# Optimization experiments

Hardware: AMD Instinct MI355X
Metric: run time of the kernel (lower is better)

The kernel has to match this reference:

```python
import jax, jax.numpy as jnp
from jax import lax
import numpy as np

DC = 3.79
HSTEP = 0.1
EPS = 1e-5
BIG = 1e10

def conv1(x, K):
    p = (K.shape[-1] - 1) // 2
    return lax.conv_general_dilated(x, K, (1,), [(p, p)], dimension_numbers=("NCH", "OIH", "NCH"))

def conv1T(x, K):
    # conv_transpose1d(stride=1, padding=p) == conv1d with flipped kernel and swapped in/out channels
    return conv1(x, jnp.flip(jnp.swapaxes(K, 0, 1), -1))

def masked_instance_norm(x, mask, eps=EPS):
    denom = jnp.sum(mask, axis=2, keepdims=True)
    mean = jnp.sum(x * mask, axis=2, keepdims=True) / denom
    meanm = mean * mask  # original multiplies the broadcast mean by the mask
    var = jnp.sum(((x - meanm) * mask) ** 2, axis=2, keepdims=True) / denom
    return (x - meanm) / jnp.sqrt(var + eps)

def avg_pool3s2(x):
    # torch avg_pool1d(kernel=3, stride=2, padding=1, count_include_pad=True)
    s = lax.reduce_window(x, 0.0, lax.add, (1, 1, 3), (1, 1, 2), [(0, 0), (0, 0), (1, 1)])
    return s / 3.0

def dist_constraint(X, M_fixed, M_padding, dc=DC):
    # X: [nb,3,n]; M_fixed, M_padding: [nb,1,n]. Vectorized (scan) version of the
    # original per-segment python loops: left/right propagation from fixed anchors
    # via unit-step (length dc) cumulative sums, blended by distance weights.
    dX = X[:, :, 1:] - X[:, :, :-1]
    d = jnp.sum(dX * dX, axis=1, keepdims=True)  # [nb,1,n-1]
    avM = jnp.floor((M_padding[..., 1:] + M_padding[..., :-1]) / 2.0) < 0.5
    dXn = dX / jnp.sqrt(d + avM) * jnp.where(avM, 0.0, dc)  # [nb,3,n-1]
    fixed = M_fixed[:, 0, :] == 1  # [nb,n]

    Xt = jnp.moveaxis(X, 2, 0)      # [n,nb,3]
    dXnt = jnp.moveaxis(dXn, 2, 0)  # [n-1,nb,3]
    ft = fixed.T                    # [n,nb]

    def lstep(carry, inp):
        prev, seen, wl = carry
        xj, dxn, fj = inp
        val = jnp.where(fj[:, None] | ~seen[:, None], xj, prev + dxn)
        wl2 = (wl + 1.0) * (~fj)
        return (val, seen | fj, wl2), (val, wl2)

    wl0 = jnp.where(ft[0], 0.0, BIG)
    _, (lv, lw) = lax.scan(lstep, (Xt[0], ft[0], wl0), (Xt[1:], dXnt, ft[1:]))
    Xleft = jnp.concatenate([X[:, :, :1], jnp.moveaxis(lv, 0, 2)], axis=2)
    wl = jnp.concatenate([wl0[:, None], lw.T], axis=1)  # [nb,n]

    def rstep(carry, inp):
        nxt, seen, wr = carry
        xj, dxn, fj = inp
        val = jnp.where(fj[:, None] | ~seen[:, None], xj, nxt - dxn)
        wr2 = (wr + 1.0) * (~fj)
        return (val, seen | fj, wr2), (val, wr2)

    wrN = jnp.where(ft[-1], 0.0, BIG)
    _, (rv, rw) = lax.scan(rstep, (Xt[-1], ft[-1], wrN), (Xt[:-1], dXnt, ft[:-1]), reverse=True)
    Xright = jnp.concatenate([jnp.moveaxis(rv, 0, 2), X[:, :, -1:]], axis=2)
    wr = jnp.concatenate([rw.T, wrN[:, None]], axis=1)

    ws = wl + wr
    ws_safe = jnp.where(ws == 0.0, 1.0, ws)
    cl = jnp.where(ws == 0.0, 0.5, wr / ws_safe)  # weight on Xleft = (wsum-wl)/wsum
    cr = jnp.where(ws == 0.0, 0.5, wl / ws_safe)
    X2 = Xleft * cl[:, None, :] + Xright * cr[:, None, :]
    return X2 * M_padding

def tr2dist(Y):
    # pairwise Euclidean distances from coords [nb,3,n] -> [nb,n,n]
    Z = jnp.swapaxes(Y, 1, 2)
    Z = Z - jnp.mean(Z, axis=1, keepdims=True)
    sq = jnp.sum(Z * Z, axis=2)
    D2 = sq[:, :, None] + sq[:, None, :] - 2.0 * jnp.einsum("bic,bjc->bij", Z, Z)
    return jnp.sqrt(jnp.maximum(D2, 0.0) + 1e-8)

def vnet_forward(x, mask, Ks, W):
    coords = x[:, -4:-1, :]
    mask_coords = jnp.repeat((x[:, -1, :] == 1)[:, None, :], 3, axis=1)
    m = mask[:, None, :]
    nL = len(Ks)
    xc = jax.nn.relu(masked_instance_norm(conv1(x, Ks[0]) * m, m))  # dropout_p=0 -> identity
    xS, mS = [], []
    for i in range(1, nL):
        K = Ks[i]
        if K.shape[0] == K.shape[1]:
            z = jax.nn.relu(masked_instance_norm(conv1(xc, K) * m, m))
            xc = xc - HSTEP * (conv1T(z, K) * m)
        else:
            xS.append(xc)
            xc = jax.nn.relu(masked_instance_norm(conv1(xc, K) * m, m))
            mS.append(m)
            m = (avg_pool3s2(m) >= 0.5).astype(x.dtype)
            xc = avg_pool3s2(xc) * m
    ns = len(xS)
    for i in reversed(range(1, nL)):
        K = Ks[i]
        if K.shape[0] == K.shape[1]:
            z = jax.nn.relu(masked_instance_norm(conv1T(xc, K) * m, m))
            xc = xc - HSTEP * (conv1(z, K) * m)
        else:
            ns -= 1
            m = mS[ns]
            xc = jnp.repeat(xc, 2, axis=-1) * m  # F.interpolate(scale=2, mode='nearest')
            z = masked_instance_norm(conv1T(xc, K) * m, m)
            xc = jax.nn.relu(z) + xS[ns]
    xc = conv1(xc, W) * m
    xc = jnp.where(mask_coords, coords, xc)
    xout = dist_constraint(xc, mask_coords[:, :1, :].astype(x.dtype), m)
    return tr2dist(xout), xout

def setup_inputs() -> dict:
    key = jax.random.key(0)
    ks = jax.random.split(key, 12)
    nb, n = 8, 2048
    feats = jax.random.normal(ks[0], (nb, 20, n), dtype=jnp.float32)
    coords = jax.random.normal(ks[1], (nb, 3, n), dtype=jnp.float32)
    lengths = jax.random.randint(ks[2], (nb,), n // 2, n + 1)
    mask = (jnp.arange(n)[None, :] < lengths[:, None]).astype(jnp.float32)  # ragged padding mask
    flag = (jax.random.uniform(ks[3], (nb, n)) < 0.5).astype(jnp.float32) * mask  # fixed-coord flag
    x = jnp.concatenate([feats, coords, flag[:, None, :]], axis=1)

    def unif(k, shape, stdv):
        return jax.random.uniform(k, shape, jnp.float32, -stdv, stdv)

    K0 = unif(ks[4], (32, 24, 3), 0.1 * 24 / 32)
    K1 = unif(ks[5], (32, 32, 3), 0.01)
    K2 = unif(ks[6], (32, 32, 3), 0.01)
    K3 = unif(ks[7], (64, 32, 3), 0.1 * 32 / 64)
    K4 = unif(ks[8], (64, 64, 3), 0.01)
    K5 = unif(ks[9], (64, 64, 3), 0.01)
    K6 = unif(ks[10], (128, 64, 3), 0.1 * 64 / 128)
    W = 0.1 * jax.random.normal(ks[11], (3, 32, 1), dtype=jnp.float32)
    return {"x": x, "mask": mask, "K0": K0, "K1": K1, "K2": K2, "K3": K3, "K4": K4, "K5": K5, "K6": K6, "W": W}

def reference(x, mask, K0, K1, K2, K3, K4, K5, K6, W):
    dists, xout = vnet_forward(x, mask, [K0, K1, K2, K3, K4, K5, K6], W)
    return (dists, xout)
```

## Files before the change

### kernel.cpp

```cpp
#include <hip/hip_runtime.h>
#include <math.h>

#define HSTEP 0.1f
#define EPS_IN 1e-5f
#define BIGF 1e10f
#define DCF 3.79f

__device__ inline float block_sum1(float v, float* sred) {
    #pragma unroll
    for (int off = 32; off > 0; off >>= 1) v += __shfl_down(v, off);
    int wid = threadIdx.x >> 6;
    int nw  = blockDim.x >> 6;
    if ((threadIdx.x & 63) == 0) sred[wid] = v;
    __syncthreads();
    float total = 0.f;
    for (int i = 0; i < nw; ++i) total += sred[i];
    __syncthreads();
    return total;
}

__device__ inline float2 block_sum2(float a, float b, float2* sred) {
    #pragma unroll
    for (int off = 32; off > 0; off >>= 1) {
        a += __shfl_down(a, off);
        b += __shfl_down(b, off);
    }
    int wid = threadIdx.x >> 6;
    int nw  = blockDim.x >> 6;
    if ((threadIdx.x & 63) == 0) sred[wid] = make_float2(a, b);
    __syncthreads();
    float ta = 0.f, tb = 0.f;
    for (int i = 0; i < nw; ++i) { ta += sred[i].x; tb += sred[i].y; }
    __syncthreads();
    return make_float2(ta, tb);
}

template<int CIN, bool TR>
__global__ void __launch_bounds__(1024)
conv_in_relu_kernel(const float* __restrict__ xin, float* __restrict__ out,
                    const float* __restrict__ K, int Cout, int N,
                    const float* __restrict__ mask, const float* __restrict__ denom,
                    const float* __restrict__ skip)
{
    __shared__ float srow[2048];
    __shared__ float swt[CIN * 3];
    __shared__ float2 sred[16];

    const int b   = blockIdx.x / Cout;
    const int co  = blockIdx.x % Cout;
    const int tid = threadIdx.x;

    for (int i = tid; i < CIN * 3; i += blockDim.x) {
        int ci = i / 3, k = i % 3;
        swt[i] = TR ? K[((size_t)ci * Cout + co) * 3 + (2 - k)]
                    : K[((size_t)co * CIN + ci) * 3 + k];
    }
    __syncthreads();

    const float* mrow = mask + (size_t)b * N;
    const float* xb   = xin + (size_t)b * CIN * N;
    float lsum = 0.f, lss = 0.f;
    for (int n = tid; n < N; n += 1024) {
        float acc = 0.f;
        const float* xr = xb + n;
        #pragma unroll 8
        for (int ci = 0; ci < CIN; ++ci, xr += N) {
            float xm = (n > 0)     ? xr[-1] : 0.f;
            float x0 = xr[0];
            float xp = (n < N - 1) ? xr[1]  : 0.f;
            acc = fmaf(swt[ci * 3 + 0], xm, acc);
            acc = fmaf(swt[ci * 3 + 1], x0, acc);
            acc = fmaf(swt[ci * 3 + 2], xp, acc);
        }
        float v = acc * mrow[n];
        srow[n] = v;
        lsum += v;
        lss  += v * v;
    }
    float dn = denom[b];
    float2 s = block_sum2(lsum, lss, sred);
    float mean = s.x / dn;
    float var  = s.y / dn - mean * mean;
    float inv  = 1.f / sqrtf(var + EPS_IN);

    float* orow = out + ((size_t)b * Cout + co) * N;
    const float* skrow = skip ? skip + ((size_t)b * Cout + co) * N : nullptr;
    for (int n = tid; n < N; n += 1024) {
        float mk = mrow[n];
        float zv = (srow[n] - mean * mk) * inv;
        float r  = fmaxf(zv, 0.f);
        if (skrow) r += skrow[n];
        orow[n] = r;
    }
}

template<int CIN, bool TR>
__global__ void __launch_bounds__(1024)
conv_axpy_kernel(const float* __restrict__ z, float* __restrict__ xc,
                 const float* __restrict__ K, int Cout, int N,
                 const float* __restrict__ mask)
{
    __shared__ float swt[CIN * 3];
    const int b   = blockIdx.x / Cout;
    const int co  = blockIdx.x % Cout;
    const int tid = threadIdx.x;

    for (int i = tid; i < CIN * 3; i += blockDim.x) {
        int ci = i / 3, k = i % 3;
        swt[i] = TR ? K[((size_t)ci * Cout + co) * 3 + (2 - k)]
                    : K[((size_t)co * CIN + ci) * 3 + k];
    }
    __syncthreads();

    const float* mrow = mask + (size_t)b * N;
    const float* zb   = z + (size_t)b * CIN * N;
    float* orow = xc + ((size_t)b * Cout + co) * N;
    for (int n = tid; n < N; n += 1024) {
        float acc = 0.f;
        const float* zr = zb + n;
        #pragma unroll 8
        for (int ci = 0; ci < CIN; ++ci, zr += N) {
            float xm = (n > 0)     ? zr[-1] : 0.f;
            float x0 = zr[0];
            float xp = (n < N - 1) ? zr[1]  : 0.f;
            acc = fmaf(swt[ci * 3 + 0], xm, acc);
            acc = fmaf(swt[ci * 3 + 1], x0, acc);
            acc = fmaf(swt[ci * 3 + 2], xp, acc);
        }
        orow[n] -= HSTEP * acc * mrow[n];
    }
}

__global__ void __launch_bounds__(256)
mask_prep_kernel(const float* __restrict__ mask, float* __restrict__ M1,
                 float* __restrict__ M2, float* __restrict__ d0, float* __restrict__ d1)
{
    __shared__ float sm1[1024];
    __shared__ float sredf[4];
    int b = blockIdx.x, tid = threadIdx.x;
    const float* mr = mask + (size_t)b * 2048;

    float s0 = 0.f;
    for (int n = tid; n < 2048; n += 256) s0 += mr[n];
    float t0 = block_sum1(s0, sredf);
    if (tid == 0) d0[b] = t0;

    for (int n = tid; n < 1024; n += 256) {
        float s = mr[2 * n];
        if (2 * n - 1 >= 0)   s += mr[2 * n - 1];
        if (2 * n + 1 < 2048) s += mr[2 * n + 1];
        float v = (s * (1.f / 3.f) >= 0.5f) ? 1.f : 0.f;
        sm1[n] = v;
        M1[(size_t)b * 1024 + n] = v;
    }
    __syncthreads();
    float s1 = 0.f;
    for (int n = tid; n < 1024; n += 256) s1 += sm1[n];
    float t1 = block_sum1(s1, sredf);
    if (tid == 0) d1[b] = t1;

    for (int n = tid; n < 512; n += 256) {
        float s = sm1[2 * n];
        if (2 * n - 1 >= 0)   s += sm1[2 * n - 1];
        if (2 * n + 1 < 1024) s += sm1[2 * n + 1];
        M2[(size_t)b * 512 + n] = (s * (1.f / 3.f) >= 0.5f) ? 1.f : 0.f;
    }
}

__global__ void pool_x_kernel(const float* __restrict__ xin, float* __restrict__ xout,
                              const float* __restrict__ mnew, int C, int Nin, int Nout, int B)
{
    int idx = blockIdx.x * blockDim.x + threadIdx.x;
    if (idx >= B * C * Nout) return;
    int n  = idx % Nout;
    int bc = idx / Nout;
    int b  = bc / C;
    const float* r = xin + (size_t)bc * Nin;
    float s = r[2 * n];
    if (2 * n - 1 >= 0)  s += r[2 * n - 1];
    if (2 * n + 1 < Nin) s += r[2 * n + 1];
    xout[idx] = s * (1.f / 3.f) * mnew[(size_t)b * Nout + n];
}

__global__ void upsample_kernel(const float* __restrict__ xin, float* __restrict__ xout,
                                const float* __restrict__ mask, int C, int Nout, int B)
{
    int idx = blockIdx.x * blockDim.x + threadIdx.x;
    if (idx >= B * C * Nout) return;
    int n  = idx % Nout;
    int bc = idx / Nout;
    int b  = bc / C;
    xout[idx] = xin[(size_t)bc * (Nout / 2) + (n >> 1)] * mask[(size_t)b * Nout + n];
}

__global__ void __launch_bounds__(1024)
dc_all_kernel(const float* __restrict__ xc32, const float* __restrict__ x,
              const float* __restrict__ W, const float* __restrict__ mask,
              const float* __restrict__ den, float* __restrict__ xout, int N)
{
    __shared__ float sX[3][2048];
    __shared__ float sD[3][2048];
    __shared__ float sM[2048];
    __shared__ unsigned long long smk[32];
    __shared__ float sW[96];

    const int b = blockIdx.x, tid = threadIdx.x;
    if (tid < 96) sW[tid] = W[tid];
    __syncthreads();

    const float* xb      = xc32 + (size_t)b * 32 * N;
    const float* flagrow = x + ((size_t)b * 24 + 23) * N;

    #pragma unroll
    for (int r = 0; r < 2; ++r) {
        int n = tid + r * 1024;
        float mk = mask[(size_t)b * N + n];
        float fl = flagrow[n];
        float v0 = 0.f, v1 = 0.f, v2 = 0.f;
        #pragma unroll 8
        for (int ci = 0; ci < 32; ++ci) {
            float xv = xb[(size_t)ci * N + n];
            v0 = fmaf(sW[0 * 32 + ci], xv, v0);
            v1 = fmaf(sW[1 * 32 + ci], xv, v1);
            v2 = fmaf(sW[2 * 32 + ci], xv, v2);
        }
        v0 *= mk; v1 *= mk; v2 *= mk;
        bool fixed = (fl == 1.f);
        if (fixed) {
            v0 = x[((size_t)b * 24 + 20) * N + n];
            v1 = x[((size_t)b * 24 + 21) * N + n];
            v2 = x[((size_t)b * 24 + 22) * N + n];
        }
        sX[0][n] = v0; sX[1][n] = v1; sX[2][n] = v2; sM[n] = mk;
        unsigned long long bm = __ballot(fixed);
        if ((tid & 63) == 0) smk[n >> 6] = bm;
    }
    __syncthreads();

    #pragma unroll
    for (int r = 0; r < 2; ++r) {
        int n = tid + r * 1024;
        if (n < N - 1) {
            float d0 = sX[0][n + 1] - sX[0][n];
            float d1 = sX[1][n + 1] - sX[1][n];
            float d2 = sX[2][n + 1] - sX[2][n];
            float d  = d0 * d0 + d1 * d1 + d2 * d2;
            bool avM = floorf((sM[n] + sM[n + 1]) * 0.5f) < 0.5f;
            if (avM) {
                sD[0][n] = 0.f; sD[1][n] = 0.f; sD[2][n] = 0.f;
            } else {
                float sq = sqrtf(d);
                sD[0][n] = (d0 / sq) * DCF;
                sD[1][n] = (d1 / sq) * DCF;
                sD[2][n] = (d2 / sq) * DCF;
            }
        }
    }
    __syncthreads();

    int len = (int)den[b];

    #pragma unroll
    for (int r = 0; r < 2; ++r) {
        int j  = tid + r * 1024;
        int cc = j >> 6, jl = j & 63;

        unsigned long long below = smk[cc] & (~0ull >> (63 - jl));
        int p = -1;
        if (below) p = (cc << 6) + 63 - __clzll(below);
        else {
            for (int c2 = cc - 1; c2 >= 0; --c2) {
                unsigned long long m = smk[c2];
                if (m) { p = (c2 << 6) + 63 - __clzll(m); break; }
            }
        }
        float l0, l1, l2, wl;
        if (p >= 0) {
            wl = (float)(j - p);
            l0 = sX[0][p]; l1 = sX[1][p]; l2 = sX[2][p];
            int kend = min(j, len - 1);
            for (int k = p; k < kend; ++k) {
                l0 += sD[0][k]; l1 += sD[1][k]; l2 += sD[2][k];
            }
        } else { wl = BIGF; l0 = sX[0][j]; l1 = sX[1][j]; l2 = sX[2][j]; }

        unsigned long long above = smk[cc] & (~0ull << jl);
        int q = -1;
        if (above) q = (cc << 6) + __ffsll((unsigned long long)above) - 1;
        else {
            for (int c2 = cc + 1; c2 < 32; ++c2) {
                unsigned long long m = smk[c2];
                if (m) { q = (c2 << 6) + __ffsll((unsigned long long)m) - 1; break; }
            }
        }
        float r0, r1, r2, wr;
        if (q >= 0) {
            wr = (float)(q - j);
            r0 = sX[0][q]; r1 = sX[1][q]; r2 = sX[2][q];
            for (int k = q - 1; k >= j; --k) {
                r0 -= sD[0][k]; r1 -= sD[1][k]; r2 -= sD[2][k];
            }
        } else { wr = BIGF; r0 = sX[0][j]; r1 = sX[1][j]; r2 = sX[2][j]; }

        float ws_ = wl + wr;
        float cl, cr;
        if (ws_ == 0.f) { cl = 0.5f; cr = 0.5f; }
        else            { cl = wr / ws_; cr = wl / ws_; }
        float mk = sM[j];
        xout[((size_t)b * 3 + 0) * N + j] = (l0 * cl + r0 * cr) * mk;
        xout[((size_t)b * 3 + 1) * N + j] = (l1 * cl + r1 * cr) * mk;
        xout[((size_t)b * 3 + 2) * N + j] = (l2 * cl + r2 * cr) * mk;
    }
}

__global__ void __launch_bounds__(256)
tr2dist_kernel(const float* __restrict__ Y, float* __restrict__ out, int B, int N)
{
    int i = blockIdx.x % N;
    int b = blockIdx.x / N;
    const float* yb = Y + (size_t)b * 3 * N;
    float y0 = yb[i], y1 = yb[N + i], y2 = yb[2 * N + i];
    float* orow = out + ((size_t)b * N + i) * N;
    for (int j = threadIdx.x; j < N; j += blockDim.x) {
        float d0 = y0 - yb[j];
        float d1 = y1 - yb[N + j];
        float d2 = y2 - yb[2 * N + j];
        orow[j] = sqrtf(fmaf(d0, d0, fmaf(d1, d1, d2 * d2)) + 1e-8f);
    }
}

extern "C" void kernel_launch(void* const* d_in, const int* in_sizes, int n_in,
                              void* d_out, int out_size, void* d_ws, size_t ws_size,
                              hipStream_t stream)
{
    const float* x    = (const float*)d_in[0];
    const float* mask = (const float*)d_in[1];
    const float* K0   = (const float*)d_in[2];
    const float* K1   = (const float*)d_in[3];
    const float* K2   = (const float*)d_in[4];
    const float* K3   = (const float*)d_in[5];
    const float* K4   = (const float*)d_in[6];
    const float* K5   = (const float*)d_in[7];
    const float* K6   = (const float*)d_in[8];
    const float* W    = (const float*)d_in[9];
    float* out = (float*)d_out;
    float* ws  = (float*)d_ws;

    const int B = 8, N = 2048;
    size_t off = 0;
    auto alloc = [&](size_t nf) { float* p = ws + off; off += nf; return p; };

    float* M1   = alloc((size_t)B * 1024);
    float* M2   = alloc((size_t)B * 512);
    float* DEN0 = alloc(8);
    float* DEN1 = alloc(8);
    float* BUF0 = alloc(1048576);
    float* BUF1 = alloc(1048576);
    float* BUF2 = alloc(1048576);
    float* BUF3 = alloc(1048576);
    (void)ws_size; (void)in_sizes; (void)n_in; (void)out_size;

    auto cdiv = [](int a, int b_) { return (a + b_ - 1) / b_; };
    float* XOUT = out + (size_t)B * N * N;

    mask_prep_kernel<<<8, 256, 0, stream>>>(mask, M1, M2, DEN0, DEN1);

    conv_in_relu_kernel<24, false><<<B * 32, 1024, 0, stream>>>(x, BUF0, K0, 32, 2048, mask, DEN0, nullptr);

    conv_in_relu_kernel<32, false><<<B * 32, 1024, 0, stream>>>(BUF0, BUF1, K1, 32, 2048, mask, DEN0, nullptr);
    conv_axpy_kernel<32, true><<<B * 32, 1024, 0, stream>>>(BUF1, BUF0, K1, 32, 2048, mask);
    conv_in_relu_kernel<32, false><<<B * 32, 1024, 0, stream>>>(BUF0, BUF1, K2, 32, 2048, mask, DEN0, nullptr);
    conv_axpy_kernel<32, true><<<B * 32, 1024, 0, stream>>>(BUF1, BUF0, K2, 32, 2048, mask);

    conv_in_relu_kernel<32, false><<<B * 64, 1024, 0, stream>>>(BUF0, BUF1, K3, 64, 2048, mask, DEN0, nullptr);
    pool_x_kernel<<<cdiv(B * 64 * 1024, 256), 256, 0, stream>>>(BUF1, BUF2, M1, 64, 2048, 1024, B);

    conv_in_relu_kernel<64, false><<<B * 64, 1024, 0, stream>>>(BUF2, BUF1, K4, 64, 1024, M1, DEN1, nullptr);
    conv_axpy_kernel<64, true><<<B * 64, 1024, 0, stream>>>(BUF1, BUF2, K4, 64, 1024, M1);
    conv_in_relu_kernel<64, false><<<B * 64, 1024, 0, stream>>>(BUF2, BUF1, K5, 64, 1024, M1, DEN1, nullptr);
    conv_axpy_kernel<64, true><<<B * 64, 1024, 0, stream>>>(BUF1, BUF2, K5, 64, 1024, M1);

    conv_in_relu_kernel<64, false><<<B * 128, 1024, 0, stream>>>(BUF2, BUF1, K6, 128, 1024, M1, DEN1, nullptr);
    pool_x_kernel<<<cdiv(B * 128 * 512, 256), 256, 0, stream>>>(BUF1, BUF3, M2, 128, 1024, 512, B);

    upsample_kernel<<<cdiv(B * 128 * 1024, 256), 256, 0, stream>>>(BUF3, BUF1, M1, 128, 1024, B);
    conv_in_relu_kernel<128, true><<<B * 64, 1024, 0, stream>>>(BUF1, BUF3, K6, 64, 1024, M1, DEN1, BUF2);

    conv_in_relu_kernel<64, true><<<B * 64, 1024, 0, stream>>>(BUF3, BUF1, K5, 64, 1024, M1, DEN1, nullptr);
    conv_axpy_kernel<64, false><<<B * 64, 1024, 0, stream>>>(BUF1, BUF3, K5, 64, 1024, M1);
    conv_in_relu_kernel<64, true><<<B * 64, 1024, 0, stream>>>(BUF3, BUF1, K4, 64, 1024, M1, DEN1, nullptr);
    conv_axpy_kernel<64, false><<<B * 64, 1024, 0, stream>>>(BUF1, BUF3, K4, 64, 1024, M1);

    upsample_kernel<<<cdiv(B * 64 * 2048, 256), 256, 0, stream>>>(BUF3, BUF1, mask, 64, 2048, B);
    conv_in_relu_kernel<64, true><<<B * 32, 1024, 0, stream>>>(BUF1, BUF2, K3, 32, 2048, mask, DEN0, BUF0);

    conv_in_relu_kernel<32, true><<<B * 32, 1024, 0, stream>>>(BUF2, BUF1, K2, 32, 2048, mask, DEN0, nullptr);
    conv_axpy_kernel<32, false><<<B * 32, 1024, 0, stream>>>(BUF1, BUF2, K2, 32, 2048, mask);
    conv_in_relu_kernel<32, true><<<B * 32, 1024, 0, stream>>>(BUF2, BUF1, K1, 32, 2048, mask, DEN0, nullptr);
    conv_axpy_kernel<32, false><<<B * 32, 1024, 0, stream>>>(BUF1, BUF2, K1, 32, 2048, mask);

    dc_all_kernel<<<B, 1024, 0, stream>>>(BUF2, x, W, mask, DEN0, XOUT, N);

    tr2dist_kernel<<<B * N, 256, 0, stream>>>(XOUT, out, B, N);
}
```

Baseline: 422.4 us.

## Fuse whole VNet forward into one cooperative persistent kernel with grid syncs

Replaces roughly 30 separate kernel launches with a single cooperative kernel of 256 blocks that runs every conv stage, pooling, upsampling, the distance constraint and the pairwise-distance output, separated by grid-wide syncs. Pooling and upsampling are folded into the neighbouring conv stages. Each thread now computes four outputs with float4 loads, and masks are kept in shared memory. This removes launch overhead and intermediate buffer traffic, at the cost of grid-sync latency, lower per-stage parallelism, and the distance-constraint stage running on only one block per batch.

```diff
diff --git a/kernel.cpp b/kernel.cpp
--- a/kernel.cpp
+++ b/kernel.cpp
@@ -1,268 +1,182 @@
 #include <hip/hip_runtime.h>
+#include <hip/hip_cooperative_groups.h>
 #include <math.h>
+
+namespace cg = cooperative_groups;
 
 #define HSTEP 0.1f
 #define EPS_IN 1e-5f
 #define BIGF 1e10f
 #define DCF 3.79f
 
-__device__ inline float block_sum1(float v, float* sred) {
+
+template<bool UPS, bool AXPY>
+__device__ void conv_stage(const float* __restrict__ in_b, float* __restrict__ out_b,
+                           const float* __restrict__ Kw, bool TR,
+                           int Cin, int Cout, int Ns,
+                           const float* __restrict__ mlds, float den,
+                           const float* __restrict__ skip_b,
+                           float* __restrict__ pool_b, const float* __restrict__ mhalf,
+                           int c, int tid,
+                           float* s_wt, float* s_red, float* s_row)
+{
+    const int T    = Ns >> 2;
+    const int P    = (T == 512) ? 1 : 2;
+    const int iters = (Cout >> 5) / P;
+    const int grp  = (P == 2) ? (tid >> 8) : 0;
+    const int tsub = (P == 2) ? (tid & 255) : tid;
+    float* swt = s_wt + grp * 384;
+    const int srcw = UPS ? (Ns >> 1) : Ns;
+
+    for (int it = 0; it < iters; ++it) {
+        const int co = c + 32 * (grp + P * it);
+        for (int i = tsub; i < Cin * 3; i += T) {
+            int ci = i / 3, k = i % 3;
+            swt[i] = TR ? Kw[((size_t)ci * Cout + co) * 3 + (2 - k)]
+                        : Kw[((size_t)co * Cin + ci) * 3 + k];
+        }
+        __syncthreads();
+
+        const int n0 = tsub * 4;
+        float a0 = 0.f, a1 = 0.f, a2 = 0.f, a3 = 0.f;
+        #pragma unroll 4
+        for (int ci = 0; ci < Cin; ++ci) {
+            const float* src = in_b + (size_t)ci * srcw;
+            float xl, x0, x1, x2, x3, xr;
+            if (!UPS) {
+                const float4 v = *(const float4*)(src + n0);
+                x0 = v.x; x1 = v.y; x2 = v.z; x3 = v.w;
+                xl = (n0 > 0)      ? src[n0 - 1] : 0.f;
+                xr = (n0 + 4 < Ns) ? src[n0 + 4] : 0.f;
+            } else {
+                const float2 s = *(const float2*)(src + (n0 >> 1));
+                x0 = s.x * mlds[n0];     x1 = s.x * mlds[n0 + 1];
+                x2 = s.y * mlds[n0 + 2]; x3 = s.y * mlds[n0 + 3];
+                xl = (n0 > 0)      ? src[(n0 - 1) >> 1] * mlds[n0 - 1] : 0.f;
+                xr = (n0 + 4 < Ns) ? src[(n0 + 4) >> 1] * mlds[n0 + 4] : 0.f;
+            }
+            const float w0 = swt[ci * 3], w1 = swt[ci * 3 + 1], w2 = swt[ci * 3 + 2];
+            a0 = fmaf(w0, xl, fmaf(w1, x0, fmaf(w2, x1, a0)));
+            a1 = fmaf(w0, x0, fmaf(w1, x1, fmaf(w2, x2, a1)));
+            a2 = fmaf(w0, x1, fmaf(w1, x2, fmaf(w2, x3, a2)));
+            a3 = fmaf(w0, x2, fmaf(w1, x3, fmaf(w2, xr, a3)));
+        }
+        const float m0 = mlds[n0], m1 = mlds[n0 + 1], m2 = mlds[n0 + 2], m3 = mlds[n0 + 3];
+        float v0 = a0 * m0, v1 = a1 * m1, v2 = a2 * m2, v3 = a3 * m3;
+        float* orow = out_b ? out_b + (size_t)co * Ns + n0 : nullptr;
+
+        if constexpr (AXPY) {
+            float4 cur = *(const float4*)orow;
+            float4 rr;
+            rr.x = cur.x - HSTEP * v0; rr.y = cur.y - HSTEP * v1;
+            rr.z = cur.z - HSTEP * v2; rr.w = cur.w - HSTEP * v3;
+            *(float4*)orow = rr;
+        } else {
+            float ls = v0 + v1 + v2 + v3;
+            float lq = v0 * v0 + v1 * v1 + v2 * v2 + v3 * v3;
+            #pragma unroll
+            for (int off = 32; off > 0; off >>= 1) {
+                ls += __shfl_down(ls, off);
+                lq += __shfl_down(lq, off);
+            }
+            const int wig = tsub >> 6;
+            const int wpg = T >> 6;
+            if ((tsub & 63) == 0) { s_red[grp * 16 + wig * 2] = ls; s_red[grp * 16 + wig * 2 + 1] = lq; }
+            __syncthreads();
+            float ts = 0.f, tq = 0.f;
+            for (int i2 = 0; i2 < wpg; ++i2) { ts += s_red[grp * 16 + i2 * 2]; tq += s_red[grp * 16 + i2 * 2 + 1]; }
+            const float mean = ts / den;
+            const float inv  = 1.f / sqrtf(tq / den - mean * mean + EPS_IN);
+            float r0 = fmaxf((v0 - mean * m0) * inv, 0.f);
+            float r1 = fmaxf((v1 - mean * m1) * inv, 0.f);
+            float r2 = fmaxf((v2 - mean * m2) * inv, 0.f);
+            float r3 = fmaxf((v3 - mean * m3) * inv, 0.f);
+            if (skip_b) {
+                const float4 sk = *(const float4*)(skip_b + (size_t)co * Ns + n0);
+                r0 += sk.x; r1 += sk.y; r2 += sk.z; r3 += sk.w;
+            }
+            if (orow) {
+                float4 rr; rr.x = r0; rr.y = r1; rr.z = r2; rr.w = r3;
+                *(float4*)orow = rr;
+            }
+            if (pool_b) {
+                float* srow = s_row + grp * 2048;
+                srow[n0] = r0; srow[n0 + 1] = r1; srow[n0 + 2] = r2; srow[n0 + 3] = r3;
+                __syncthreads();
+                const int Nh = Ns >> 1;
+                if (tsub < (T >> 1)) {
+                    const int np0 = tsub * 4;
+                    float zm1 = (np0 > 0) ? srow[2 * np0 - 1] : 0.f;
+                    float4 p;
+                    p.x = (zm1 + srow[2*np0] + srow[2*np0+1]) * (1.f/3.f) * mhalf[np0];
+                    p.y = (srow[2*np0+1] + srow[2*np0+2] + srow[2*np0+3]) * (1.f/3.f) * mhalf[np0+1];
+                    p.z = (srow[2*np0+3] + srow[2*np0+4] + srow[2*np0+5]) * (1.f/3.f) * mhalf[np0+2];
+                    p.w = (srow[2*np0+5] + srow[2*np0+6] + srow[2*np0+7]) * (1.f/3.f) * mhalf[np0+3];
+                    *(float4*)(pool_b + (size_t)co * Nh + np0) = p;
+                }
+            }
+        }
+        __syncthreads();
+    }
+}
+
+__device__ void dc_stage(const float* __restrict__ xc32, const float* __restrict__ x,
+                         const float* __restrict__ Wg, float* __restrict__ xout,
+                         int b, int tid, const float* sm_mask, float den0,
+                         float* ub, unsigned long long* smk, float* sW)
+{
+    const int N = 2048;
+    float* sX0 = ub;         float* sX1 = ub + 2048;  float* sX2 = ub + 4096;
+    float* sD0 = ub + 6144;  float* sD1 = ub + 8192;  float* sD2 = ub + 10240;
+    if (tid < 96) sW[tid] = Wg[tid];
+    __syncthreads();
+    const float* flagrow = x + ((size_t)b * 24 + 23) * N;
+    const float* cxr = x + ((size_t)b * 24 + 20) * N;
+    const float* cyr = x + ((size_t)b * 24 + 21) * N;
+    const float* czr = x + ((size_t)b * 24 + 22) * N;
+
     #pragma unroll
-    for (int off = 32; off > 0; off >>= 1) v += __shfl_down(v, off);
-    int wid = threadIdx.x >> 6;
-    int nw  = blockDim.x >> 6;
-    if ((threadIdx.x & 63) == 0) sred[wid] = v;
-    __syncthreads();
-    float total = 0.f;
-    for (int i = 0; i < nw; ++i) total += sred[i];
-    __syncthreads();
-    return total;
-}
-
-__device__ inline float2 block_sum2(float a, float b, float2* sred) {
-    #pragma unroll
-    for (int off = 32; off > 0; off >>= 1) {
-        a += __shfl_down(a, off);
-        b += __shfl_down(b, off);
-    }
-    int wid = threadIdx.x >> 6;
-    int nw  = blockDim.x >> 6;
-    if ((threadIdx.x & 63) == 0) sred[wid] = make_float2(a, b);
-    __syncthreads();
-    float ta = 0.f, tb = 0.f;
-    for (int i = 0; i < nw; ++i) { ta += sred[i].x; tb += sred[i].y; }
-    __syncthreads();
-    return make_float2(ta, tb);
-}
-
-template<int CIN, bool TR>
-__global__ void __launch_bounds__(1024)
-conv_in_relu_kernel(const float* __restrict__ xin, float* __restrict__ out,
-                    const float* __restrict__ K, int Cout, int N,
-                    const float* __restrict__ mask, const float* __restrict__ denom,
-                    const float* __restrict__ skip)
-{
-    __shared__ float srow[2048];
-    __shared__ float swt[CIN * 3];
-    __shared__ float2 sred[16];
-
-    const int b   = blockIdx.x / Cout;
-    const int co  = blockIdx.x % Cout;
-    const int tid = threadIdx.x;
-
-    for (int i = tid; i < CIN * 3; i += blockDim.x) {
-        int ci = i / 3, k = i % 3;
-        swt[i] = TR ? K[((size_t)ci * Cout + co) * 3 + (2 - k)]
-                    : K[((size_t)co * CIN + ci) * 3 + k];
-    }
-    __syncthreads();
-
-    const float* mrow = mask + (size_t)b * N;
-    const float* xb   = xin + (size_t)b * CIN * N;
-    float lsum = 0.f, lss = 0.f;
-    for (int n = tid; n < N; n += 1024) {
-        float acc = 0.f;
-        const float* xr = xb + n;
-        #pragma unroll 8
-        for (int ci = 0; ci < CIN; ++ci, xr += N) {
-            float xm = (n > 0)     ? xr[-1] : 0.f;
-            float x0 = xr[0];
-            float xp = (n < N - 1) ? xr[1]  : 0.f;
-            acc = fmaf(swt[ci * 3 + 0], xm, acc);
-            acc = fmaf(swt[ci * 3 + 1], x0, acc);
-            acc = fmaf(swt[ci * 3 + 2], xp, acc);
-        }
-        float v = acc * mrow[n];
-        srow[n] = v;
-        lsum += v;
-        lss  += v * v;
-    }
-    float dn = denom[b];
-    float2 s = block_sum2(lsum, lss, sred);
-    float mean = s.x / dn;
-    float var  = s.y / dn - mean * mean;
-    float inv  = 1.f / sqrtf(var + EPS_IN);
-
-    float* orow = out + ((size_t)b * Cout + co) * N;
-    const float* skrow = skip ? skip + ((size_t)b * Cout + co) * N : nullptr;
-    for (int n = tid; n < N; n += 1024) {
-        float mk = mrow[n];
-        float zv = (srow[n] - mean * mk) * inv;
-        float r  = fmaxf(zv, 0.f);
-        if (skrow) r += skrow[n];
-        orow[n] = r;
-    }
-}
-
-template<int CIN, bool TR>
-__global__ void __launch_bounds__(1024)
-conv_axpy_kernel(const float* __restrict__ z, float* __restrict__ xc,
-                 const float* __restrict__ K, int Cout, int N,
-                 const float* __restrict__ mask)
-{
-    __shared__ float swt[CIN * 3];
-    const int b   = blockIdx.x / Cout;
-    const int co  = blockIdx.x % Cout;
-    const int tid = threadIdx.x;
-
-    for (int i = tid; i < CIN * 3; i += blockDim.x) {
-        int ci = i / 3, k = i % 3;
-        swt[i] = TR ? K[((size_t)ci * Cout + co) * 3 + (2 - k)]
-                    : K[((size_t)co * CIN + ci) * 3 + k];
-    }
-    __syncthreads();
-
-    const float* mrow = mask + (size_t)b * N;
-    const float* zb   = z + (size_t)b * CIN * N;
-    float* orow = xc + ((size_t)b * Cout + co) * N;
-    for (int n = tid; n < N; n += 1024) {
-        float acc = 0.f;
-        const float* zr = zb + n;
-        #pragma unroll 8
-        for (int ci = 0; ci < CIN; ++ci, zr += N) {
-            float xm = (n > 0)     ? zr[-1] : 0.f;
-            float x0 = zr[0];
-            float xp = (n < N - 1) ? zr[1]  : 0.f;
-            acc = fmaf(swt[ci * 3 + 0], xm, acc);
-            acc = fmaf(swt[ci * 3 + 1], x0, acc);
-            acc = fmaf(swt[ci * 3 + 2], xp, acc);
-        }
-        orow[n] -= HSTEP * acc * mrow[n];
-    }
-}
-
-__global__ void __launch_bounds__(256)
-mask_prep_kernel(const float* __restrict__ mask, float* __restrict__ M1,
-                 float* __restrict__ M2, float* __restrict__ d0, float* __restrict__ d1)
-{
-    __shared__ float sm1[1024];
-    __shared__ float sredf[4];
-    int b = blockIdx.x, tid = threadIdx.x;
-    const float* mr = mask + (size_t)b * 2048;
-
-    float s0 = 0.f;
-    for (int n = tid; n < 2048; n += 256) s0 += mr[n];
-    float t0 = block_sum1(s0, sredf);
-    if (tid == 0) d0[b] = t0;
-
-    for (int n = tid; n < 1024; n += 256) {
-        float s = mr[2 * n];
-        if (2 * n - 1 >= 0)   s += mr[2 * n - 1];
-        if (2 * n + 1 < 2048) s += mr[2 * n + 1];
-        float v = (s * (1.f / 3.f) >= 0.5f) ? 1.f : 0.f;
-        sm1[n] = v;
-        M1[(size_t)b * 1024 + n] = v;
-    }
-    __syncthreads();
-    float s1 = 0.f;
-    for (int n = tid; n < 1024; n += 256) s1 += sm1[n];
-    float t1 = block_sum1(s1, sredf);
-    if (tid == 0) d1[b] = t1;
-
-    for (int n = tid; n < 512; n += 256) {
-        float s = sm1[2 * n];
-        if (2 * n - 1 >= 0)   s += sm1[2 * n - 1];
-        if (2 * n + 1 < 1024) s += sm1[2 * n + 1];
-        M2[(size_t)b * 512 + n] = (s * (1.f / 3.f) >= 0.5f) ? 1.f : 0.f;
-    }
-}
-
-__global__ void pool_x_kernel(const float* __restrict__ xin, float* __restrict__ xout,
-                              const float* __restrict__ mnew, int C, int Nin, int Nout, int B)
-{
-    int idx = blockIdx.x * blockDim.x + threadIdx.x;
-    if (idx >= B * C * Nout) return;
-    int n  = idx % Nout;
-    int bc = idx / Nout;
-    int b  = bc / C;
-    const float* r = xin + (size_t)bc * Nin;
-    float s = r[2 * n];
-    if (2 * n - 1 >= 0)  s += r[2 * n - 1];
-    if (2 * n + 1 < Nin) s += r[2 * n + 1];
-    xout[idx] = s * (1.f / 3.f) * mnew[(size_t)b * Nout + n];
-}
-
-__global__ void upsample_kernel(const float* __restrict__ xin, float* __restrict__ xout,
-                                const float* __restrict__ mask, int C, int Nout, int B)
-{
-    int idx = blockIdx.x * blockDim.x + threadIdx.x;
-    if (idx >= B * C * Nout) return;
-    int n  = idx % Nout;
-    int bc = idx / Nout;
-    int b  = bc / C;
-    xout[idx] = xin[(size_t)bc * (Nout / 2) + (n >> 1)] * mask[(size_t)b * Nout + n];
-}
-
-__global__ void __launch_bounds__(1024)
-dc_all_kernel(const float* __restrict__ xc32, const float* __restrict__ x,
-              const float* __restrict__ W, const float* __restrict__ mask,
-              const float* __restrict__ den, float* __restrict__ xout, int N)
-{
-    __shared__ float sX[3][2048];
-    __shared__ float sD[3][2048];
-    __shared__ float sM[2048];
-    __shared__ unsigned long long smk[32];
-    __shared__ float sW[96];
-
-    const int b = blockIdx.x, tid = threadIdx.x;
-    if (tid < 96) sW[tid] = W[tid];
-    __syncthreads();
-
-    const float* xb      = xc32 + (size_t)b * 32 * N;
-    const float* flagrow = x + ((size_t)b * 24 + 23) * N;
-
-    #pragma unroll
-    for (int r = 0; r < 2; ++r) {
-        int n = tid + r * 1024;
-        float mk = mask[(size_t)b * N + n];
+    for (int r = 0; r < 4; ++r) {
+        int n = tid + r * 512;
+        float mk = sm_mask[n];
         float fl = flagrow[n];
         float v0 = 0.f, v1 = 0.f, v2 = 0.f;
         #pragma unroll 8
         for (int ci = 0; ci < 32; ++ci) {
-            float xv = xb[(size_t)ci * N + n];
-            v0 = fmaf(sW[0 * 32 + ci], xv, v0);
-            v1 = fmaf(sW[1 * 32 + ci], xv, v1);
-            v2 = fmaf(sW[2 * 32 + ci], xv, v2);
+            float xv = xc32[(size_t)ci * N + n];
+            v0 = fmaf(sW[ci], xv, v0);
+            v1 = fmaf(sW[32 + ci], xv, v1);
+            v2 = fmaf(sW[64 + ci], xv, v2);
         }
         v0 *= mk; v1 *= mk; v2 *= mk;
         bool fixed = (fl == 1.f);
-        if (fixed) {
-            v0 = x[((size_t)b * 24 + 20) * N + n];
-            v1 = x[((size_t)b * 24 + 21) * N + n];
-            v2 = x[((size_t)b * 24 + 22) * N + n];
-        }
-        sX[0][n] = v0; sX[1][n] = v1; sX[2][n] = v2; sM[n] = mk;
+        if (fixed) { v0 = cxr[n]; v1 = cyr[n]; v2 = czr[n]; }
+        sX0[n] = v0; sX1[n] = v1; sX2[n] = v2;
         unsigned long long bm = __ballot(fixed);
         if ((tid & 63) == 0) smk[n >> 6] = bm;
     }
     __syncthreads();
 
     #pragma unroll
-    for (int r = 0; r < 2; ++r) {
-        int n = tid + r * 1024;
+    for (int r = 0; r < 4; ++r) {
+        int n = tid + r * 512;
         if (n < N - 1) {
-            float d0 = sX[0][n + 1] - sX[0][n];
-            float d1 = sX[1][n + 1] - sX[1][n];
-            float d2 = sX[2][n + 1] - sX[2][n];
+            float d0 = sX0[n+1] - sX0[n], d1 = sX1[n+1] - sX1[n], d2 = sX2[n+1] - sX2[n];
             float d  = d0 * d0 + d1 * d1 + d2 * d2;
-            bool avM = floorf((sM[n] + sM[n + 1]) * 0.5f) < 0.5f;
-            if (avM) {
-                sD[0][n] = 0.f; sD[1][n] = 0.f; sD[2][n] = 0.f;
-            } else {
+            bool avM = floorf((sm_mask[n] + sm_mask[n + 1]) * 0.5f) < 0.5f;
+            if (avM) { sD0[n] = 0.f; sD1[n] = 0.f; sD2[n] = 0.f; }
+            else {
                 float sq = sqrtf(d);
-                sD[0][n] = (d0 / sq) * DCF;
-                sD[1][n] = (d1 / sq) * DCF;
-                sD[2][n] = (d2 / sq) * DCF;
+                sD0[n] = (d0 / sq) * DCF; sD1[n] = (d1 / sq) * DCF; sD2[n] = (d2 / sq) * DCF;
             }
         }
     }
     __syncthreads();
 
-    int len = (int)den[b];
-
+    int len = (int)den0;
     #pragma unroll
-    for (int r = 0; r < 2; ++r) {
-        int j  = tid + r * 1024;
+    for (int r = 0; r < 4; ++r) {
+        int j  = tid + r * 512;
         int cc = j >> 6, jl = j & 63;
 
         unsigned long long below = smk[cc] & (~0ull >> (63 - jl));
@@ -277,56 +191,173 @@
         float l0, l1, l2, wl;
         if (p >= 0) {
             wl = (float)(j - p);
-            l0 = sX[0][p]; l1 = sX[1][p]; l2 = sX[2][p];
+            l0 = sX0[p]; l1 = sX1[p]; l2 = sX2[p];
             int kend = min(j, len - 1);
-            for (int k = p; k < kend; ++k) {
-                l0 += sD[0][k]; l1 += sD[1][k]; l2 += sD[2][k];
-            }
-        } else { wl = BIGF; l0 = sX[0][j]; l1 = sX[1][j]; l2 = sX[2][j]; }
+            for (int k = p; k < kend; ++k) { l0 += sD0[k]; l1 += sD1[k]; l2 += sD2[k]; }
+        } else { wl = BIGF; l0 = sX0[j]; l1 = sX1[j]; l2 = sX2[j]; }
 
         unsigned long long above = smk[cc] & (~0ull << jl);
         int q = -1;
-        if (above) q = (cc << 6) + __ffsll((unsigned long long)above) - 1;
+        if (above) q = (cc << 6) + __ffsll(above) - 1;
         else {
             for (int c2 = cc + 1; c2 < 32; ++c2) {
                 unsigned long long m = smk[c2];
-                if (m) { q = (c2 << 6) + __ffsll((unsigned long long)m) - 1; break; }
+                if (m) { q = (c2 << 6) + __ffsll(m) - 1; break; }
             }
         }
         float r0, r1, r2, wr;
         if (q >= 0) {
             wr = (float)(q - j);
-            r0 = sX[0][q]; r1 = sX[1][q]; r2 = sX[2][q];
-            for (int k = q - 1; k >= j; --k) {
-                r0 -= sD[0][k]; r1 -= sD[1][k]; r2 -= sD[2][k];
-            }
-        } else { wr = BIGF; r0 = sX[0][j]; r1 = sX[1][j]; r2 = sX[2][j]; }
-
-        float ws_ = wl + wr;
-        float cl, cr;
+            r0 = sX0[q]; r1 = sX1[q]; r2 = sX2[q];
+            for (int k = q - 1; k >= j; --k) { r0 -= sD0[k]; r1 -= sD1[k]; r2 -= sD2[k]; }
+        } else { wr = BIGF; r0 = sX0[j]; r1 = sX1[j]; r2 = sX2[j]; }
+
+        float ws_ = wl + wr, cl, cr;
         if (ws_ == 0.f) { cl = 0.5f; cr = 0.5f; }
         else            { cl = wr / ws_; cr = wl / ws_; }
-        float mk = sM[j];
-        xout[((size_t)b * 3 + 0) * N + j] = (l0 * cl + r0 * cr) * mk;
-        xout[((size_t)b * 3 + 1) * N + j] = (l1 * cl + r1 * cr) * mk;
-        xout[((size_t)b * 3 + 2) * N + j] = (l2 * cl + r2 * cr) * mk;
+        float mk = sm_mask[j];
+        xout[j]         = (l0 * cl + r0 * cr) * mk;
+        xout[N + j]     = (l1 * cl + r1 * cr) * mk;
+        xout[2 * N + j] = (l2 * cl + r2 * cr) * mk;
     }
 }
 
-__global__ void __launch_bounds__(256)
-tr2dist_kernel(const float* __restrict__ Y, float* __restrict__ out, int B, int N)
+__global__ void __launch_bounds__(512, 1)
+vnet_all(const float* __restrict__ x, const float* __restrict__ mask,
+         const float* __restrict__ K0, const float* __restrict__ K1,
+         const float* __restrict__ K2, const float* __restrict__ K3,
+         const float* __restrict__ K4, const float* __restrict__ K5,
+         const float* __restrict__ K6, const float* __restrict__ W,
+         float* __restrict__ out, float* __restrict__ B0, float* __restrict__ B1,
+         float* __restrict__ B2, float* __restrict__ B3)
 {
-    int i = blockIdx.x % N;
-    int b = blockIdx.x / N;
-    const float* yb = Y + (size_t)b * 3 * N;
-    float y0 = yb[i], y1 = yb[N + i], y2 = yb[2 * N + i];
-    float* orow = out + ((size_t)b * N + i) * N;
-    for (int j = threadIdx.x; j < N; j += blockDim.x) {
-        float d0 = y0 - yb[j];
-        float d1 = y1 - yb[N + j];
-        float d2 = y2 - yb[2 * N + j];
-        orow[j] = sqrtf(fmaf(d0, d0, fmaf(d1, d1, d2 * d2)) + 1e-8f);
-    }
+    __shared__ __align__(16) float sm_mask[2048];
+    __shared__ __align__(16) float sm_M1[1024];
+    __shared__ __align__(16) float sm_M2[512];
+    __shared__ float s_wt[2 * 384];
+    __shared__ float s_red[32];
+    __shared__ __align__(16) float s_row[2 * 2048];
+    __shared__ float s_den[2];
+    __shared__ __align__(16) float ubig[12288];
+    __shared__ unsigned long long smk[32];
+    __shared__ float sWl[96];
+
+    cg::grid_group grid = cg::this_grid();
+    const int g = blockIdx.x, tid = threadIdx.x;
+    const int b = g >> 5, c = g & 31;
+
+    {
+        const float* mrow = mask + (size_t)b * 2048;
+        *(float4*)(sm_mask + tid * 4) = *(const float4*)(mrow + tid * 4);
+        __syncthreads();
+        if (tid < 256) {
+            int np0 = tid * 4;
+            #pragma unroll
+            for (int k = 0; k < 4; ++k) {
+                int np = np0 + k;
+                float s = sm_mask[2 * np];
+                if (2 * np - 1 >= 0)   s += sm_mask[2 * np - 1];
+                if (2 * np + 1 < 2048) s += sm_mask[2 * np + 1];
+                sm_M1[np] = (s * (1.f / 3.f) >= 0.5f) ? 1.f : 0.f;
+            }
+        }
+        __syncthreads();
+        if (tid < 128) {
+            int np0 = tid * 4;
+            #pragma unroll
+            for (int k = 0; k < 4; ++k) {
+                int np = np0 + k;
+                float s = sm_M1[2 * np];
+                if (2 * np - 1 >= 0)   s += sm_M1[2 * np - 1];
+                if (2 * np + 1 < 1024) s += sm_M1[2 * np + 1];
+                sm_M2[np] = (s * (1.f / 3.f) >= 0.5f) ? 1.f : 0.f;
+            }
+        }
+        __syncthreads();
+        float l0 = sm_mask[tid*4] + sm_mask[tid*4+1] + sm_mask[tid*4+2] + sm_mask[tid*4+3];
+        float l1 = sm_M1[tid * 2] + sm_M1[tid * 2 + 1];
+        #pragma unroll
+        for (int off = 32; off > 0; off >>= 1) { l0 += __shfl_down(l0, off); l1 += __shfl_down(l1, off); }
+        if ((tid & 63) == 0) { s_red[(tid >> 6) * 2] = l0; s_red[(tid >> 6) * 2 + 1] = l1; }
+        __syncthreads();
+        if (tid == 0) {
+            float t0 = 0.f, t1 = 0.f;
+            for (int i = 0; i < 8; ++i) { t0 += s_red[i * 2]; t1 += s_red[i * 2 + 1]; }
+            s_den[0] = t0; s_den[1] = t1;
+        }
+        __syncthreads();
+    }
+    const float den0 = s_den[0], den1 = s_den[1];
+
+    const size_t S = 65536;
+    const float* xb = x + (size_t)b * 24 * 2048;
+    float* p0 = B0 + (size_t)b * S;
+    float* p1 = B1 + (size_t)b * S;
+    float* p2 = B2 + (size_t)b * S;
+    float* p3 = B3 + (size_t)b * S;
+
+    #define GS() grid.sync()
+
+    conv_stage<false,false>(xb, p0, K0, false, 24, 32, 2048, sm_mask, den0, nullptr, nullptr, nullptr, c, tid, s_wt, s_red, s_row); GS();
+    conv_stage<false,false>(p0, p1, K1, false, 32, 32, 2048, sm_mask, den0, nullptr, nullptr, nullptr, c, tid, s_wt, s_red, s_row); GS();
+    conv_stage<false,true >(p1, p0, K1, true , 32, 32, 2048, sm_mask, 1.f , nullptr, nullptr, nullptr, c, tid, s_wt, s_red, s_row); GS();
+    conv_stage<false,false>(p0, p1, K2, false, 32, 32, 2048, sm_mask, den0, nullptr, nullptr, nullptr, c, tid, s_wt, s_red, s_row); GS();
+    conv_stage<false,true >(p1, p0, K2, true , 32, 32, 2048, sm_mask, 1.f , nullptr, nullptr, nullptr, c, tid, s_wt, s_red, s_row); GS();
+    conv_stage<false,false>(p0, nullptr, K3, false, 32, 64, 2048, sm_mask, den0, nullptr, p2, sm_M1, c, tid, s_wt, s_red, s_row); GS();
+    conv_stage<false,false>(p2, p1, K4, false, 64, 64, 1024, sm_M1, den1, nullptr, nullptr, nullptr, c, tid, s_wt, s_red, s_row); GS();
+    conv_stage<false,true >(p1, p2, K4, true , 64, 64, 1024, sm_M1, 1.f , nullptr, nullptr, nullptr, c, tid, s_wt, s_red, s_row); GS();
+    conv_stage<false,false>(p2, p1, K5, false, 64, 64, 1024, sm_M1, den1, nullptr, nullptr, nullptr, c, tid, s_wt, s_red, s_row); GS();
+    conv_stage<false,true >(p1, p2, K5, true , 64, 64, 1024, sm_M1, 1.f , nullptr, nullptr, nullptr, c, tid, s_wt, s_red, s_row); GS();
+    conv_stage<false,false>(p2, nullptr, K6, false, 64, 128, 1024, sm_M1, den1, nullptr, p3, sm_M2, c, tid, s_wt, s_red, s_row); GS();
+    conv_stage<true ,false>(p3, p1, K6, true , 128, 64, 1024, sm_M1, den1, p2, nullptr, nullptr, c, tid, s_wt, s_red, s_row); GS();
+    conv_stage<false,false>(p1, p2, K5, true , 64, 64, 1024, sm_M1, den1, nullptr, nullptr, nullptr, c, tid, s_wt, s_red, s_row); GS();
+    conv_stage<false,true >(p2, p1, K5, false, 64, 64, 1024, sm_M1, 1.f , nullptr, nullptr, nullptr, c, tid, s_wt, s_red, s_row); GS();
+    conv_stage<false,false>(p1, p2, K4, true , 64, 64, 1024, sm_M1, den1, nullptr, nullptr, nullptr, c, tid, s_wt, s_red, s_row); GS();
+    conv_stage<false,true >(p2, p1, K4, false, 64, 64, 1024, sm_M1, 1.f , nullptr, nullptr, nullptr, c, tid, s_wt, s_red, s_row); GS();
+    conv_stage<true ,false>(p1, p2, K3, true , 64, 32, 2048, sm_mask, den0, p0, nullptr, nullptr, c, tid, s_wt, s_red, s_row); GS();
+    conv_stage<false,false>(p2, p1, K2, true , 32, 32, 2048, sm_mask, den0, nullptr, nullptr, nullptr, c, tid, s_wt, s_red, s_row); GS();
+    conv_stage<false,true >(p1, p2, K2, false, 32, 32, 2048, sm_mask, 1.f , nullptr, nullptr, nullptr, c, tid, s_wt, s_red, s_row); GS();
+    conv_stage<false,false>(p2, p1, K1, true , 32, 32, 2048, sm_mask, den0, nullptr, nullptr, nullptr, c, tid, s_wt, s_red, s_row); GS();
+    conv_stage<false,true >(p1, p2, K1, false, 32, 32, 2048, sm_mask, 1.f , nullptr, nullptr, nullptr, c, tid, s_wt, s_red, s_row); GS();
+
+    float* xout = out + (size_t)8 * 2048 * 2048 + (size_t)b * 3 * 2048;
+    if (c == 0) dc_stage(p2, x, W, xout, b, tid, sm_mask, den0, ubig, smk, sWl);
+    GS();
+
+    {
+        float* y = ubig;
+        #pragma unroll
+        for (int i = 0; i < 3; ++i)
+            *(float4*)(y + tid * 4 + i * 2048) = *(const float4*)(xout + tid * 4 + i * 2048);
+        __syncthreads();
+        const int j0 = tid * 4;
+        const float4 w0 = *(const float4*)(y + j0);
+        const float4 w1 = *(const float4*)(y + 2048 + j0);
+        const float4 w2 = *(const float4*)(y + 4096 + j0);
+        for (int r = 0; r < 64; ++r) {
+            const int i = c * 64 + r;
+            const float a0 = y[i], a1 = y[2048 + i], a2 = y[4096 + i];
+            float4 o;
+            {
+                float d0 = a0 - w0.x, d1 = a1 - w1.x, d2 = a2 - w2.x;
+                o.x = sqrtf(fmaf(d0, d0, fmaf(d1, d1, fmaf(d2, d2, 1e-8f))));
+            }
+            {
+                float d0 = a0 - w0.y, d1 = a1 - w1.y, d2 = a2 - w2.y;
+                o.y = sqrtf(fmaf(d0, d0, fmaf(d1, d1, fmaf(d2, d2, 1e-8f))));
+            }
+            {
+                float d0 = a0 - w0.z, d1 = a1 - w1.z, d2 = a2 - w2.z;
+                o.z = sqrtf(fmaf(d0, d0, fmaf(d1, d1, fmaf(d2, d2, 1e-8f))));
+            }
+            {
+                float d0 = a0 - w0.w, d1 = a1 - w1.w, d2 = a2 - w2.w;
+                o.w = sqrtf(fmaf(d0, d0, fmaf(d1, d1, fmaf(d2, d2, 1e-8f))));
+            }
+            *(float4*)(out + ((size_t)b * 2048 + i) * 2048 + j0) = o;
+        }
+    }
+    #undef GS
 }
 
 extern "C" void kernel_launch(void* const* d_in, const int* in_sizes, int n_in,
@@ -345,61 +376,19 @@
     const float* W    = (const float*)d_in[9];
     float* out = (float*)d_out;
     float* ws  = (float*)d_ws;
-
-    const int B = 8, N = 2048;
-    size_t off = 0;
-    auto alloc = [&](size_t nf) { float* p = ws + off; off += nf; return p; };
-
-    float* M1   = alloc((size_t)B * 1024);
-    float* M2   = alloc((size_t)B * 512);
-    float* DEN0 = alloc(8);
-    float* DEN1 = alloc(8);
-    float* BUF0 = alloc(1048576);
-    float* BUF1 = alloc(1048576);
-    float* BUF2 = alloc(1048576);
-    float* BUF3 = alloc(1048576);
-    (void)ws_size; (void)in_sizes; (void)n_in; (void)out_size;
-
-    auto cdiv = [](int a, int b_) { return (a + b_ - 1) / b_; };
-    float* XOUT = out + (size_t)B * N * N;
-
-    mask_prep_kernel<<<8, 256, 0, stream>>>(mask, M1, M2, DEN0, DEN1);
-
-    conv_in_relu_kernel<24, false><<<B * 32, 1024, 0, stream>>>(x, BUF0, K0, 32, 2048, mask, DEN0, nullptr);
-
-    conv_in_relu_kernel<32, false><<<B * 32, 1024, 0, stream>>>(BUF0, BUF1, K1, 32, 2048, mask, DEN0, nullptr);
-    conv_axpy_kernel<32, true><<<B * 32, 1024, 0, stream>>>(BUF1, BUF0, K1, 32, 2048, mask);
-    conv_in_relu_kernel<32, false><<<B * 32, 1024, 0, stream>>>(BUF0, BUF1, K2, 32, 2048, mask, DEN0, nullptr);
-    conv_axpy_kernel<32, true><<<B * 32, 1024, 0, stream>>>(BUF1, BUF0, K2, 32, 2048, mask);
-
-    conv_in_relu_kernel<32, false><<<B * 64, 1024, 0, stream>>>(BUF0, BUF1, K3, 64, 2048, mask, DEN0, nullptr);
-    pool_x_kernel<<<cdiv(B * 64 * 1024, 256), 256, 0, stream>>>(BUF1, BUF2, M1, 64, 2048, 1024, B);
-
-    conv_in_relu_kernel<64, false><<<B * 64, 1024, 0, stream>>>(BUF2, BUF1, K4, 64, 1024, M1, DEN1, nullptr);
-    conv_axpy_kernel<64, true><<<B * 64, 1024, 0, stream>>>(BUF1, BUF2, K4, 64, 1024, M1);
-    conv_in_relu_kernel<64, false><<<B * 64, 1024, 0, stream>>>(BUF2, BUF1, K5, 64, 1024, M1, DEN1, nullptr);
-    conv_axpy_kernel<64, true><<<B * 64, 1024, 0, stream>>>(BUF1, BUF2, K5, 64, 1024, M1);
-
-    conv_in_relu_kernel<64, false><<<B * 128, 1024, 0, stream>>>(BUF2, BUF1, K6, 128, 1024, M1, DEN1, nullptr);
-    pool_x_kernel<<<cdiv(B * 128 * 512, 256), 256, 0, stream>>>(BUF1, BUF3, M2, 128, 1024, 512, B);
-
-    upsample_kernel<<<cdiv(B * 128 * 1024, 256), 256, 0, stream>>>(BUF3, BUF1, M1, 128, 1024, B);
-    conv_in_relu_kernel<128, true><<<B * 64, 1024, 0, stream>>>(BUF1, BUF3, K6, 64, 1024, M1, DEN1, BUF2);
-
-    conv_in_relu_kernel<64, true><<<B * 64, 1024, 0, stream>>>(BUF3, BUF1, K5, 64, 1024, M1, DEN1, nullptr);
-    conv_axpy_kernel<64, false><<<B * 64, 1024, 0, stream>>>(BUF1, BUF3, K5, 64, 1024, M1);
-    conv_in_relu_kernel<64, true><<<B * 64, 1024, 0, stream>>>(BUF3, BUF1, K4, 64, 1024, M1, DEN1, nullptr);
-    conv_axpy_kernel<64, false><<<B * 64, 1024, 0, stream>>>(BUF1, BUF3, K4, 64, 1024, M1);
-
-    upsample_kernel<<<cdiv(B * 64 * 2048, 256), 256, 0, stream>>>(BUF3, BUF1, mask, 64, 2048, B);
-    conv_in_relu_kernel<64, true><<<B * 32, 1024, 0, stream>>>(BUF1, BUF2, K3, 32, 2048, mask, DEN0, BUF0);
-
-    conv_in_relu_kernel<32, true><<<B * 32, 1024, 0, stream>>>(BUF2, BUF1, K2, 32, 2048, mask, DEN0, nullptr);
-    conv_axpy_kernel<32, false><<<B * 32, 1024, 0, stream>>>(BUF1, BUF2, K2, 32, 2048, mask);
-    conv_in_relu_kernel<32, true><<<B * 32, 1024, 0, stream>>>(BUF2, BUF1, K1, 32, 2048, mask, DEN0, nullptr);
-    conv_axpy_kernel<32, false><<<B * 32, 1024, 0, stream>>>(BUF1, BUF2, K1, 32, 2048, mask);
-
-    dc_all_kernel<<<B, 1024, 0, stream>>>(BUF2, x, W, mask, DEN0, XOUT, N);
-
-    tr2dist_kernel<<<B * N, 256, 0, stream>>>(XOUT, out, B, N);
+    (void)in_sizes; (void)n_in; (void)out_size; (void)ws_size;
+
+    const size_t S = 65536;
+    float* B0 = ws;
+    float* B1 = ws + 8 * S;
+    float* B2 = ws + 16 * S;
+    float* B3 = ws + 24 * S;
+
+    void* args[] = {
+        (void*)&x, (void*)&mask, (void*)&K0, (void*)&K1, (void*)&K2, (void*)&K3,
+        (void*)&K4, (void*)&K5, (void*)&K6, (void*)&W,
+        (void*)&out, (void*)&B0, (void*)&B1, (void*)&B2, (void*)&B3
+    };
+    hipLaunchCooperativeKernel((const void*)vnet_all, dim3(256), dim3(512),
+                               args, 0, stream);
 }
```

New measurement: 1.138 ms. 2.69x slower.
